# Optimization experiments

Measured on AMD Instinct MI355X. Metric: run time of the kernel, lower is better.

## Reference

```python
import jax, jax.numpy as jnp
import numpy as np

K = 3  # filter_size
PAD = (K - 1) // 2


def setup_inputs() -> dict:
    key = jax.random.key(0)
    k1, k2, k3 = jax.random.split(key, 3)
    B, C, H, Wd = 4, 256, 128, 128
    x = jax.random.normal(k1, (B, C, H, Wd), dtype=jnp.float32)
    # 1x1 conv params: out_channels = C * K^2
    W = jax.random.normal(k2, (C * K * K, C), dtype=jnp.float32) * (1.0 / np.sqrt(C))
    b = jax.random.normal(k3, (C * K * K,), dtype=jnp.float32) * 0.01
    return {"x": x, "W": W, "b": b}


def _extract_patches(x):
    # x: (B,C,H,W) -> (B,C,H,W,K*K), kernel positions row-major (matches F.unfold)
    B, C, H, Wd = x.shape
    xp = jnp.pad(x, ((0, 0), (0, 0), (PAD, PAD), (PAD, PAD)))
    patches = jnp.stack(
        [xp[:, :, i:i + H, j:j + Wd] for i in range(K) for j in range(K)],
        axis=-1,
    )
    return patches


def reference(x, W, b):
    B, C, H, Wd = x.shape
    # 1x1 conv: (B,C,H,W) x (C*K^2, C) -> (B, C*K^2, H, W)
    filters = jnp.einsum('bchw,oc->bohw', x, W) + b[None, :, None, None]
    # view(B, C, K^2, H, W) then permute to (B,C,H,W,K^2)
    filters = filters.reshape(B, C, K * K, H, Wd).transpose(0, 1, 3, 4, 2)
    patches = _extract_patches(x)  # (B,C,H,W,K^2), unfold ordering c-major then pos
    return jnp.sum(patches * filters, axis=-1)  # (B,C,H,W)
```

## Files before the change

kernel.cpp:

```cpp
#include <hip/hip_runtime.h>


typedef __attribute__((ext_vector_type(8))) short bf16x8;
typedef __attribute__((ext_vector_type(4))) float f32x4;

__device__ __forceinline__ unsigned int f2bf(float f) {
    unsigned int u = __float_as_uint(f);
    return (u + 0x7fffu + ((u >> 16) & 1u)) >> 16;
}
__device__ __forceinline__ unsigned int pack2(float a, float b) {
    return f2bf(a) | (f2bf(b) << 16);
}

__global__ __launch_bounds__(256) void wconv_kernel(const float* __restrict__ W,
                                                    unsigned char* __restrict__ Wb) {
    int idx0 = blockIdx.x * 256 + threadIdx.x;
    int o = idx0 >> 5, g = idx0 & 31;
    const float4* src = (const float4*)(W + ((size_t)o << 8) + ((size_t)g << 3));
    float4 v0 = src[0], v1 = src[1];
    uint4 pk;
    pk.x = pack2(v0.x, v0.y); pk.y = pack2(v0.z, v0.w);
    pk.z = pack2(v1.x, v1.y); pk.w = pack2(v1.z, v1.w);
    int kh = g >> 4, g2 = g & 15, s = g2 >> 2, kq = g2 & 3;
    int chunk = o / 144, oc = o - chunk * 144;
    int c_local = oc / 9, p = oc - c_local * 9;
    int q = c_local >> 2, c4 = c_local & 3;
    int idx = c4 * 9 + p;
    int ni = idx >> 2, j = idx & 3, r = (q << 2) + j;
    int jsub = kh * 3 + ni / 3, ni_ = ni % 3;
    size_t dst = (size_t)chunk * 73728 + (size_t)jsub * 12288
               + (size_t)(s * 3 + ni_) * 1024 + (size_t)((kq << 4) + r) * 16;
    *(uint4*)(Wb + dst) = pk;
}


#define SYNC_VM(N) asm volatile("s_waitcnt vmcnt(" #N ") lgkmcnt(0)\n\ts_barrier" ::: "memory")
#define SYNC_LG    asm volatile("s_waitcnt lgkmcnt(0)\n\ts_barrier" ::: "memory")
#define FENCE      asm volatile("" ::: "memory")

#define STAGE(CH, J)                                                            \
    do {                                                                        \
        const int sl_ = (wv < 6) ? wv : (wv - 6);                               \
        const unsigned char* bs_ = Wb + (size_t)(CH) * 73728                    \
            + (size_t)(J) * 12288 + sl_ * 2048 + (lane << 4);                   \
        unsigned char* bd_ = smem + ((J) % 4) * 12288 + sl_ * 2048;             \
        __builtin_amdgcn_global_load_lds(                                       \
            (const __attribute__((address_space(1))) void*)(bs_),               \
            (__attribute__((address_space(3))) void*)(bd_), 16, 0, 0);          \
        __builtin_amdgcn_global_load_lds(                                       \
            (const __attribute__((address_space(1))) void*)(bs_ + 1024),        \
            (__attribute__((address_space(3))) void*)(bd_ + 1024), 16, 0, 0);   \
    } while (0)

#define MFMA_SUB(J)                                                             \
    do {                                                                        \
        const int kh_ = (J) / 3, snib_ = ((J) % 3) * 3;                         \
        const unsigned char* bb_ = smem + ((J) % 4) * 12288 + (lane << 4);      \
        _Pragma("unroll")                                                       \
        for (int s_ = 0; s_ < 4; ++s_) {                                        \
            const bf16x8 a_ = afr[(kh_ << 2) + s_];                             \
            _Pragma("unroll")                                                   \
            for (int ni_ = 0; ni_ < 3; ++ni_) {                                 \
                const bf16x8 bq_ = *(const bf16x8*)(bb_ + ((s_ * 3 + ni_) << 10)); \
                acc[snib_ + ni_] = __builtin_amdgcn_mfma_f32_16x16x32_bf16(     \
                    bq_, a_, acc[snib_ + ni_], 0, 0, 0);                        \
            }                                                                   \
        }                                                                       \
    } while (0)

__global__ __launch_bounds__(512, 4) void dfgemm_kernel(
        const unsigned char* __restrict__ Wb, const float* __restrict__ x,
        const float* __restrict__ bias, float* __restrict__ out) {
    __shared__ __align__(16) unsigned char smem[49152];

    const int t = threadIdx.x;
    const int lane = t & 63, wv = t >> 6;
    const int quad = lane >> 4, lrow = lane & 15;

    const int b = blockIdx.x >> 7;
    const int h = blockIdx.x & 127;
    const int w = (wv << 4) + lrow;

    STAGE(0, 0); STAGE(0, 1); STAGE(0, 2); STAGE(0, 3);

    bf16x8 afr[8];
    {
        const float* xrow = x + ((size_t)b << 22) + (h << 7);
        #pragma unroll
        for (int gg = 0; gg < 8; ++gg) {
            const float* p = xrow + ((size_t)((gg << 5) + (quad << 3)) << 14) + w;
            float v[8];
            #pragma unroll
            for (int e = 0; e < 8; ++e) v[e] = p[(size_t)e << 14];
            uint4 pk;
            pk.x = pack2(v[0], v[1]); pk.y = pack2(v[2], v[3]);
            pk.z = pack2(v[4], v[5]); pk.w = pack2(v[6], v[7]);
            afr[gg] = *(const bf16x8*)&pk;
        }
    }
    SYNC_VM(0);

    #pragma unroll 1
    for (int chunk = 0; chunk < 16; ++chunk) {
        const int c1 = (chunk + 1) & 15;
        f32x4 acc[9];
        const f32x4 zero = {0.f, 0.f, 0.f, 0.f};
        #pragma unroll
        for (int ni = 0; ni < 9; ++ni) acc[ni] = zero;

        SYNC_VM(8);
        MFMA_SUB(0);

        SYNC_VM(8);
        STAGE(chunk, 4);
        MFMA_SUB(1);

        SYNC_VM(8);
        STAGE(chunk, 5);
        MFMA_SUB(2);

        SYNC_VM(8);
        STAGE(c1, 2);
        MFMA_SUB(3);

        SYNC_VM(4);
        STAGE(c1, 3);
        MFMA_SUB(4);

        SYNC_VM(4);
        STAGE(c1, 0);
        MFMA_SUB(5);

        SYNC_LG;
        STAGE(c1, 1);
        FENCE;

        #pragma unroll
        for (int c4 = 0; c4 < 4; ++c4) {
            const int cg = (chunk << 4) + (quad << 2) + c4;
            const float* bp = bias + cg * 9;
            const float* xc = x + ((size_t)((b << 8) + cg) << 14);
            float sum = 0.f;
            #pragma unroll
            for (int p = 0; p < 9; ++p) {
                const int idx = c4 * 9 + p;
                const int ni = idx >> 2, j = idx & 3;
                const float yv = acc[ni][j];
                const int hh = h + p / 3 - 1, ww = w + p % 3 - 1;
                float xv = 0.f;
                if ((unsigned)hh < 128u && (unsigned)ww < 128u)
                    xv = xc[(hh << 7) + ww];
                sum += (yv + bp[p]) * xv;
            }
            out[((size_t)((b << 8) + cg) << 14) + (h << 7) + w] = sum;
        }
    }
}

extern "C" void kernel_launch(void* const* d_in, const int* in_sizes, int n_in,
                              void* d_out, int out_size, void* d_ws, size_t ws_size,
                              hipStream_t stream) {
    const float* x    = (const float*)d_in[0];
    const float* W    = (const float*)d_in[1];
    const float* bias = (const float*)d_in[2];
    float* out = (float*)d_out;

    unsigned char* Wb = (unsigned char*)d_ws;

    wconv_kernel<<<288, 256, 0, stream>>>(W, Wb);
    dfgemm_kernel<<<512, 512, 0, stream>>>(Wb, x, bias, out);
}
```

Measured before the change: 206.1 us.

## Use six LDS stages, pair MFMA sub-steps, raise wave priority, swizzle blocks

Grows LDS from four to six 12KB weight slots so each sub-step owns its own buffer. The chunk loop drops from six barrier phases to three, each staging two slots and running two MFMA sub-steps between s_setprio raises. Block indices are remapped so neighbouring blocks spread across batches and rows. Bias is loaded as vectorised float4 values. The larger 72KB LDS footprint may cut the number of resident blocks per CU.

```diff
diff --git a/kernel.cpp b/kernel.cpp
--- a/kernel.cpp
+++ b/kernel.cpp
@@ -35,7 +35,6 @@
 
 
 #define SYNC_VM(N) asm volatile("s_waitcnt vmcnt(" #N ") lgkmcnt(0)\n\ts_barrier" ::: "memory")
-#define SYNC_LG    asm volatile("s_waitcnt lgkmcnt(0)\n\ts_barrier" ::: "memory")
 #define FENCE      asm volatile("" ::: "memory")
 
 #define STAGE(CH, J)                                                            \
@@ -43,7 +42,7 @@
         const int sl_ = (wv < 6) ? wv : (wv - 6);                               \
         const unsigned char* bs_ = Wb + (size_t)(CH) * 73728                    \
             + (size_t)(J) * 12288 + sl_ * 2048 + (lane << 4);                   \
-        unsigned char* bd_ = smem + ((J) % 4) * 12288 + sl_ * 2048;             \
+        unsigned char* bd_ = smem + (size_t)(J) * 12288 + sl_ * 2048;           \
         __builtin_amdgcn_global_load_lds(                                       \
             (const __attribute__((address_space(1))) void*)(bs_),               \
             (__attribute__((address_space(3))) void*)(bd_), 16, 0, 0);          \
@@ -55,7 +54,7 @@
 #define MFMA_SUB(J)                                                             \
     do {                                                                        \
         const int kh_ = (J) / 3, snib_ = ((J) % 3) * 3;                         \
-        const unsigned char* bb_ = smem + ((J) % 4) * 12288 + (lane << 4);      \
+        const unsigned char* bb_ = smem + (size_t)(J) * 12288 + (lane << 4);    \
         _Pragma("unroll")                                                       \
         for (int s_ = 0; s_ < 4; ++s_) {                                        \
             const bf16x8 a_ = afr[(kh_ << 2) + s_];                             \
@@ -71,14 +70,15 @@
 __global__ __launch_bounds__(512, 4) void dfgemm_kernel(
         const unsigned char* __restrict__ Wb, const float* __restrict__ x,
         const float* __restrict__ bias, float* __restrict__ out) {
-    __shared__ __align__(16) unsigned char smem[49152];
+    __shared__ __align__(16) unsigned char smem[73728];
 
     const int t = threadIdx.x;
     const int lane = t & 63, wv = t >> 6;
     const int quad = lane >> 4, lrow = lane & 15;
 
-    const int b = blockIdx.x >> 7;
-    const int h = blockIdx.x & 127;
+    const int swz = ((blockIdx.x & 7) << 6) + (blockIdx.x >> 3);
+    const int b = swz >> 7;
+    const int h = swz & 127;
     const int w = (wv << 4) + lrow;
 
     STAGE(0, 0); STAGE(0, 1); STAGE(0, 2); STAGE(0, 3);
@@ -108,37 +108,34 @@
         #pragma unroll
         for (int ni = 0; ni < 9; ++ni) acc[ni] = zero;
 
-        SYNC_VM(8);
-        MFMA_SUB(0);
+        SYNC_VM(4);
+        STAGE(chunk, 4); STAGE(chunk, 5);
+        __builtin_amdgcn_s_setprio(1);
+        MFMA_SUB(0); MFMA_SUB(1);
+        __builtin_amdgcn_s_setprio(0);
 
         SYNC_VM(8);
-        STAGE(chunk, 4);
-        MFMA_SUB(1);
-
-        SYNC_VM(8);
-        STAGE(chunk, 5);
-        MFMA_SUB(2);
-
-        SYNC_VM(8);
-        STAGE(c1, 2);
-        MFMA_SUB(3);
+        STAGE(c1, 0); STAGE(c1, 1);
+        __builtin_amdgcn_s_setprio(1);
+        MFMA_SUB(2); MFMA_SUB(3);
+        __builtin_amdgcn_s_setprio(0);
 
         SYNC_VM(4);
-        STAGE(c1, 3);
-        MFMA_SUB(4);
-
-        SYNC_VM(4);
-        STAGE(c1, 0);
-        MFMA_SUB(5);
-
-        SYNC_LG;
-        STAGE(c1, 1);
+        STAGE(c1, 2); STAGE(c1, 3);
+        __builtin_amdgcn_s_setprio(1);
+        MFMA_SUB(4); MFMA_SUB(5);
+        __builtin_amdgcn_s_setprio(0);
         FENCE;
 
+        float bb[36];
+        {
+            const float4* bsrc = (const float4*)(bias + ((chunk << 4) + (quad << 2)) * 9);
+            #pragma unroll
+            for (int i = 0; i < 9; ++i) *(float4*)(bb + 4 * i) = bsrc[i];
+        }
         #pragma unroll
         for (int c4 = 0; c4 < 4; ++c4) {
             const int cg = (chunk << 4) + (quad << 2) + c4;
-            const float* bp = bias + cg * 9;
             const float* xc = x + ((size_t)((b << 8) + cg) << 14);
             float sum = 0.f;
             #pragma unroll
@@ -150,7 +147,7 @@
                 float xv = 0.f;
                 if ((unsigned)hh < 128u && (unsigned)ww < 128u)
                     xv = xc[(hh << 7) + ww];
-                sum += (yv + bp[p]) * xv;
+                sum += (yv + bb[idx]) * xv;
             }
             out[((size_t)((b << 8) + cg) << 14) + (h << 7) + w] = sum;
         }
```

New measurement: 251.6 us. 1.22x slower.
